# Kernel optimization log

Hardware: AMD Instinct MI355X
Metric: run time of the kernel (lower is better)

Reference implementation:

```python
import jax, jax.numpy as jnp
import numpy as np
from functools import partial

NEG_INF = -1e30

def _alive_mask(x, umbral=0.1):
    # 3x3 max-pool (stride 1, SAME) over channel 0, compare to threshold
    m = x[..., :1]
    pooled = jax.lax.reduce_window(m, NEG_INF, jax.lax.max,
                                   (1, 3, 3, 1), (1, 1, 1, 1), 'SAME')
    return pooled > umbral

def _perception_kernel(canales):
    # identity + sobel-x + sobel-y, fixed (non-learned) depthwise filters
    identidad = np.outer(np.float32([0, 1, 0]), np.float32([0, 1, 0]))
    dx = np.float32(np.outer([1, 2, 1], [-1, 0, 1]) / 8.0)
    dy = dx.T
    k = np.stack([identidad, dx, dy], -1)            # [3,3,3]
    k = np.repeat(k[:, :, None, :], canales + 3, 2)   # [3,3,C+3,3]
    C = canales + 3
    # TF depthwise output channel order: chan*3 + multiplier -> flatten last two dims
    return jnp.asarray(k.reshape(3, 3, 1, C * 3))

def setup_inputs() -> dict:
    key = jax.random.key(0)
    ks = jax.random.split(key, 6)
    B, H, C, HID = 16, 256, 14, 256
    PERC = (C + 3) * 3  # 51
    x = jax.random.uniform(ks[0], (B, H, H, C), dtype=jnp.float32)
    imagen = jax.random.uniform(ks[1], (H, H, 3), dtype=jnp.float32)
    W1 = jax.random.normal(ks[2], (PERC, HID), dtype=jnp.float32) * 0.05
    b1 = jnp.zeros((HID,), dtype=jnp.float32)
    W2 = jax.random.normal(ks[3], (HID, C), dtype=jnp.float32) * 0.05
    b2 = jnp.zeros((C,), dtype=jnp.float32)
    return {"x": x, "imagen": imagen, "W1": W1, "b1": b1, "W2": W2, "b2": b2}

def reference(x, imagen, W1, b1, W2, b2):
    paso = 0.1
    umbral_actualizacion = 0.5
    B = x.shape[0]
    C = x.shape[-1]

    vivos_antes = _alive_mask(x)

    # percibir: concat image, fixed depthwise conv (identity/sobel)
    img_b = jnp.broadcast_to(imagen[None], (B,) + imagen.shape)
    xc = jnp.concatenate([x, img_b], axis=3)                 # [B,H,W,C+3]
    kernel = _perception_kernel(C)                            # [3,3,1,(C+3)*3]
    perc = jax.lax.conv_general_dilated(
        xc, kernel, window_strides=(1, 1), padding='SAME',
        dimension_numbers=('NHWC', 'HWIO', 'NHWC'),
        feature_group_count=C + 3)                            # [B,H,W,51]

    # pointwise MLP (1x1 convs)
    h = jax.nn.relu(jnp.einsum('bhwc,cd->bhwd', perc, W1) + b1)
    dx = (jnp.einsum('bhwd,dc->bhwc', h, W2) + b2) * paso

    # stochastic update mask
    mk = jax.random.fold_in(jax.random.key(0), 1234)
    upd = jax.random.uniform(mk, x[..., :1].shape) <= umbral_actualizacion
    x = x + dx * upd.astype(jnp.float32)

    vivos = jnp.logical_and(vivos_antes, _alive_mask(x))
    return x * vivos.astype(jnp.float32)
```

## Files before the change

kernel.cpp:

```cpp
#include <hip/hip_runtime.h>
#include <stdint.h>

#define C    14
#define CX   17
#define PERC 51
#define HID  256

typedef __attribute__((ext_vector_type(4))) short  bf16x4;
typedef __attribute__((ext_vector_type(8))) short  bf16x8;
typedef __attribute__((ext_vector_type(4))) float  f32x4;
typedef __attribute__((ext_vector_type(8))) unsigned short u16x8;
typedef __attribute__((ext_vector_type(2))) uint32_t u32x2;

__device__ __forceinline__ float bfu(unsigned short u) {
  return __uint_as_float(((uint32_t)u) << 16);
}
__device__ __forceinline__ unsigned short bf16r(float f) {
  uint32_t u = __float_as_uint(f);
  return (unsigned short)((u + 0x7fffu + ((u >> 16) & 1u)) >> 16);
}
__device__ __forceinline__ uint32_t pack2_bf16(float lo, float hi) {
  const uint32_t ul = __float_as_uint(lo) + 0x8000u;
  const uint32_t uh = __float_as_uint(hi) + 0x8000u;
#if __has_builtin(__builtin_amdgcn_perm)
  return __builtin_amdgcn_perm(uh, ul, 0x07060302u);
#else
  return (uh & 0xffff0000u) | (ul >> 16);
#endif
}
__device__ __forceinline__ unsigned short pack1_bf16(float f) {
  return (unsigned short)((__float_as_uint(f) + 0x8000u) >> 16);
}

__device__ __forceinline__ f32x4 mfma32(bf16x8 a, bf16x8 b, f32x4 c) {
  return __builtin_amdgcn_mfma_f32_16x16x32_bf16(a, b, c, 0, 0, 0);
}
#if __has_builtin(__builtin_amdgcn_mfma_f32_16x16x16bf16_1k)
#define HAVE_MFMA16_BUILTIN 1
#endif
__device__ __forceinline__ f32x4 mfma16(bf16x4 a, bf16x4 b, f32x4 c) {
#ifdef HAVE_MFMA16_BUILTIN
  return __builtin_amdgcn_mfma_f32_16x16x16bf16_1k(a, b, c, 0, 0, 0);
#else
  asm volatile("v_mfma_f32_16x16x16_bf16 %0, %1, %2, %0" : "+v"(c) : "v"(a), "v"(b));
  return c;
#endif
}

__device__ __forceinline__ void tf_round(uint32_t& x0, uint32_t& x1, int r) {
  x0 += x1; x1 = (x1 << r) | (x1 >> (32 - r)); x1 ^= x0;
}
__device__ __forceinline__ void threefry2x32(uint32_t k0, uint32_t k1,
                                             uint32_t& x0, uint32_t& x1) {
  const uint32_t ks2 = k0 ^ k1 ^ 0x1BD11BDAu;
  x0 += k0; x1 += k1;
  tf_round(x0,x1,13); tf_round(x0,x1,15); tf_round(x0,x1,26); tf_round(x0,x1,6);
  x0 += k1; x1 += ks2 + 1u;
  tf_round(x0,x1,17); tf_round(x0,x1,29); tf_round(x0,x1,16); tf_round(x0,x1,24);
  x0 += ks2; x1 += k0 + 2u;
  tf_round(x0,x1,13); tf_round(x0,x1,15); tf_round(x0,x1,26); tf_round(x0,x1,6);
  x0 += k0; x1 += k1 + 3u;
  tf_round(x0,x1,17); tf_round(x0,x1,29); tf_round(x0,x1,16); tf_round(x0,x1,24);
  x0 += k1; x1 += ks2 + 4u;
  tf_round(x0,x1,13); tf_round(x0,x1,15); tf_round(x0,x1,26); tf_round(x0,x1,6);
  x0 += ks2; x1 += k0 + 5u;
}
__device__ __forceinline__ float upd_val(uint32_t gpix) {
  uint32_t fk0 = 0u, fk1 = 1234u;
  threefry2x32(0u, 0u, fk0, fk1);
  uint32_t a = 0u, b = gpix;
  threefry2x32(fk0, fk1, a, b);
  const uint32_t bits = a ^ b;
  const float u = __uint_as_float((bits >> 9) | 0x3f800000u) - 1.0f;
  return (u <= 0.5f) ? 1.0f : 0.0f;
}

__global__ void nca_prep(const float* __restrict__ W1, const float* __restrict__ W2,
                         const float* __restrict__ b2,
                         unsigned short* __restrict__ w1fu,
                         unsigned short* __restrict__ w2fu,
                         float* __restrict__ b2p) {
  const int bid = blockIdx.x, t = threadIdx.x;
  if (bid < 64) {
    const int f = bid * 256 + t;
    const int j = f & 7, l = (f >> 3) & 63, k2 = (f >> 9) & 1, mt = f >> 10;
    const int n = mt * 16 + (l & 15);
    const int k = k2 * 32 + ((l >> 4) & 3) * 8 + j;
    const float v = (k < PERC) ? W1[k * HID + n] : 0.0f;
    w1fu[f] = bf16r(v);
  } else if (bid < 80) {
    const int f = (bid - 64) * 256 + t;
    const int j = f & 3, l = (f >> 2) & 63, ks = f >> 8;
    const int co = l & 15;
    const int k = ks * 16 + ((l >> 4) & 3) * 4 + j;
    const float v = (co < C) ? W2[k * C + co] : 0.0f;
    w2fu[f] = bf16r(v);
  } else if (t < 16) {
    b2p[t] = (t < C) ? b2[t] : 0.0f;
  }
}

__global__ __launch_bounds__(256, 2)
void nca_main(const float* __restrict__ x, const float* __restrict__ img,
              const float* __restrict__ b1,
              const unsigned short* __restrict__ w1fu,
              const unsigned short* __restrict__ w2fu,
              const float* __restrict__ b2p,
              float* __restrict__ out, float* __restrict__ plane) {
  __shared__ unsigned short xcs[18 * 18 * 24];
  __shared__ unsigned short Ps[256 * 64];
  __shared__ float updf[256];

  const int t    = threadIdx.x;
  const int bid  = blockIdx.x;
  const int bb   = bid >> 8;
  const int tile = bid & 255;
  const int row0 = (tile >> 4) << 4, col0 = (tile & 15) << 4;

  for (int e = t; e < 324; e += 256) {
    const int r = e / 18, c = e - r * 18;
    const int gr = row0 + r - 1, gc = col0 + c - 1;
    uint32_t w[8]; unsigned short w16;
    if ((unsigned)gr < 256u && (unsigned)gc < 256u) {
      const size_t gp = (size_t)bb * 65536 + (size_t)gr * 256 + gc;
      const float* xp = x + gp * C;
      float v[17];
      #pragma unroll
      for (int k = 0; k < 7; ++k) {
        const float2 f2 = *(const float2*)(xp + 2 * k);
        v[2 * k] = f2.x; v[2 * k + 1] = f2.y;
      }
      const float* ip = img + ((size_t)gr * 256 + gc) * 3;
      v[14] = ip[0]; v[15] = ip[1]; v[16] = ip[2];
      #pragma unroll
      for (int k = 0; k < 8; ++k)
        w[k] = pack2_bf16(v[2 * k], v[2 * k + 1]);
      w16 = pack1_bf16(v[16]);
    } else {
      #pragma unroll
      for (int k = 0; k < 8; ++k) w[k] = 0u;
      w16 = 0;
    }
    uint32_t* d = (uint32_t*)&xcs[e * 24];
    #pragma unroll
    for (int k = 0; k < 8; ++k) d[k] = w[k];
    xcs[e * 24 + 16] = w16;
  }

  {
    const uint32_t g = ((uint32_t)bb * 256u + (uint32_t)(row0 + (t >> 4))) * 256u
                       + (uint32_t)(col0 + (t & 15));
    updf[t] = upd_val(g);
  }
  __syncthreads();

  const int pr = t >> 4, pc = t & 15;
  float pe[64];
  #pragma unroll
  for (int h = 0; h < 2; ++h) {
    u16x8 nb[9];
    #pragma unroll
    for (int i = 0; i < 3; ++i)
      #pragma unroll
      for (int j = 0; j < 3; ++j)
        nb[i * 3 + j] = *(const u16x8*)&xcs[((pr + i) * 18 + (pc + j)) * 24 + h * 8];
    #pragma unroll
    for (int cc = 0; cc < 8; ++cc) {
      const int ch = h * 8 + cc;
      const float a00 = bfu(nb[0][cc]), a01 = bfu(nb[1][cc]), a02 = bfu(nb[2][cc]);
      const float a10 = bfu(nb[3][cc]), a11 = bfu(nb[4][cc]), a12 = bfu(nb[5][cc]);
      const float a20 = bfu(nb[6][cc]), a21 = bfu(nb[7][cc]), a22 = bfu(nb[8][cc]);
      pe[3 * ch + 0] = a11;
      pe[3 * ch + 1] = ((a02 - a00) + 2.0f * (a12 - a10) + (a22 - a20)) * 0.125f;
      pe[3 * ch + 2] = ((a20 - a00) + 2.0f * (a21 - a01) + (a22 - a02)) * 0.125f;
    }
  }
  {
    float a[9];
    #pragma unroll
    for (int i = 0; i < 3; ++i)
      #pragma unroll
      for (int j = 0; j < 3; ++j)
        a[i * 3 + j] = bfu(xcs[((pr + i) * 18 + (pc + j)) * 24 + 16]);
    pe[48] = a[4];
    pe[49] = ((a[2] - a[0]) + 2.0f * (a[5] - a[3]) + (a[8] - a[6])) * 0.125f;
    pe[50] = ((a[6] - a[0]) + 2.0f * (a[7] - a[1]) + (a[8] - a[2])) * 0.125f;
  }
  #pragma unroll
  for (int k = PERC; k < 64; ++k) pe[k] = 0.0f;
  #pragma unroll
  for (int g = 0; g < 8; ++g) {
    uint4 v;
    v.x = pack2_bf16(pe[g * 8 + 0], pe[g * 8 + 1]);
    v.y = pack2_bf16(pe[g * 8 + 2], pe[g * 8 + 3]);
    v.z = pack2_bf16(pe[g * 8 + 4], pe[g * 8 + 5]);
    v.w = pack2_bf16(pe[g * 8 + 6], pe[g * 8 + 7]);
    *(uint4*)&Ps[(t << 6) + ((g ^ (t & 7)) << 3)] = v;
  }
  __syncthreads();

  const int lane = t & 63;
  const int wv   = t >> 6;
  const int wbase = wv << 6;
  const int lg = lane >> 4;
  const int lc = lane & 15;

  bf16x8 bF0[4], bF1[4];
  #pragma unroll
  for (int nt = 0; nt < 4; ++nt) {
    const int pix = wbase + nt * 16 + lc;
    bF0[nt] = *(const bf16x8*)&Ps[(pix << 6) + ((lg ^ (pix & 7)) << 3)];
    bF1[nt] = *(const bf16x8*)&Ps[(pix << 6) + (((4 + lg) ^ (pix & 7)) << 3)];
  }

  f32x4 dxacc[4];
  {
    const float4 b2v = *(const float4*)(b2p + lg * 4);
    #pragma unroll
    for (int nt = 0; nt < 4; ++nt)
      dxacc[nt] = (f32x4){b2v.x, b2v.y, b2v.z, b2v.w};
  }

  #pragma unroll
  for (int nc = 0; nc < 4; ++nc) {
    bf16x8 aF[4][2];
    #pragma unroll
    for (int m4 = 0; m4 < 4; ++m4)
      #pragma unroll
      for (int k2 = 0; k2 < 2; ++k2)
        aF[m4][k2] = *(const bf16x8*)(w1fu + (((((nc * 4 + m4) * 2 + k2) * 64) + lane) << 3));

    f32x4 acc[4][4];
    #pragma unroll
    for (int m4 = 0; m4 < 4; ++m4) {
      const float4 b1v = *(const float4*)(b1 + nc * 64 + m4 * 16 + lg * 4);
      #pragma unroll
      for (int nt = 0; nt < 4; ++nt)
        acc[m4][nt] = (f32x4){b1v.x, b1v.y, b1v.z, b1v.w};
    }

    #pragma unroll
    for (int nt = 0; nt < 4; ++nt) {
      #pragma unroll
      for (int m4 = 0; m4 < 4; ++m4) acc[m4][nt] = mfma32(aF[m4][0], bF0[nt], acc[m4][nt]);
      #pragma unroll
      for (int m4 = 0; m4 < 4; ++m4) acc[m4][nt] = mfma32(aF[m4][1], bF1[nt], acc[m4][nt]);
    }

    #pragma unroll
    for (int m4 = 0; m4 < 4; ++m4) {
      const bf16x4 wf = *(const bf16x4*)(w2fu + ((((nc * 4 + m4) * 64) + lane) << 2));
      #pragma unroll
      for (int nt = 0; nt < 4; ++nt) {
        u32x2 pw;
        pw.x = pack2_bf16(fmaxf(acc[m4][nt][0], 0.0f), fmaxf(acc[m4][nt][1], 0.0f));
        pw.y = pack2_bf16(fmaxf(acc[m4][nt][2], 0.0f), fmaxf(acc[m4][nt][3], 0.0f));
        dxacc[nt] = mfma16(wf, __builtin_bit_cast(bf16x4, pw), dxacc[nt]);
      }
    }
  }
#ifndef HAVE_MFMA16_BUILTIN
  asm volatile("s_nop 7\n\ts_nop 7" :::);
#endif

  #pragma unroll
  for (int nt = 0; nt < 4; ++nt) {
    const int pix = wbase + nt * 16 + lc;
    const float sc = 0.1f * updf[pix];
    const int gr = row0 + (pix >> 4), gc = col0 + (pix & 15);
    const size_t gp = (size_t)bb * 65536 + (size_t)gr * 256 + gc;
    const float* xp = x + gp * C + lg * 4;
    float* op = out + gp * C + lg * 4;
    const f32x4 d = dxacc[nt];
    if (lg < 3) {
      const float2 u0 = *(const float2*)xp;
      const float2 u1 = *(const float2*)(xp + 2);
      const float r0 = u0.x + d[0] * sc, r1 = u0.y + d[1] * sc;
      const float r2 = u1.x + d[2] * sc, r3 = u1.y + d[3] * sc;
      *(float2*)op = make_float2(r0, r1);
      *(float2*)(op + 2) = make_float2(r2, r3);
      if (lg == 0) plane[gp] = r0;
    } else {
      const float2 u0 = *(const float2*)xp;
      *(float2*)op = make_float2(u0.x + d[0] * sc, u0.y + d[1] * sc);
    }
  }
}

__global__ __launch_bounds__(256)
void nca_mask(const float* __restrict__ x, const float* __restrict__ plane,
              float* __restrict__ out) {
  __shared__ float sN[18 * 18];
  __shared__ float sO[18 * 18];
  const int t    = threadIdx.x;
  const int bid  = blockIdx.x;
  const int bb   = bid >> 8;
  const int tile = bid & 255;
  const int row0 = (tile >> 4) << 4, col0 = (tile & 15) << 4;

  for (int e = t; e < 18 * 18; e += 256) {
    const int r = e / 18, c = e - r * 18;
    const int gr = row0 + r - 1, gc = col0 + c - 1;
    float vn = 0.0f, vo = 0.0f;
    if ((unsigned)gr < 256u && (unsigned)gc < 256u) {
      const size_t gp = ((size_t)bb * 256 + gr) * 256 + gc;
      vn = plane[gp];
      vo = x[gp * C];
    }
    sN[e] = vn; sO[e] = vo;
  }
  __syncthreads();

  const int pr = t >> 4, pc = t & 15;
  float mn = -1e30f, mo = -1e30f;
  #pragma unroll
  for (int i = 0; i < 3; ++i)
    #pragma unroll
    for (int j = 0; j < 3; ++j) {
      mn = fmaxf(mn, sN[(pr + i) * 18 + pc + j]);
      mo = fmaxf(mo, sO[(pr + i) * 18 + pc + j]);
    }
  const bool alive = (mo > 0.1f) && (mn > 0.1f);
  if (!alive) {
    const size_t gp = ((size_t)bb * 256 + row0 + pr) * 256 + col0 + pc;
    float* __restrict__ o = out + gp * C;
    const float2 z = make_float2(0.0f, 0.0f);
    #pragma unroll
    for (int k = 0; k < 7; ++k) ((float2*)o)[k] = z;
  }
}

extern "C" void kernel_launch(void* const* d_in, const int* in_sizes, int n_in,
                              void* d_out, int out_size, void* d_ws, size_t ws_size,
                              hipStream_t stream) {
  const float* x  = (const float*)d_in[0];
  const float* im = (const float*)d_in[1];
  const float* W1 = (const float*)d_in[2];
  const float* b1 = (const float*)d_in[3];
  const float* W2 = (const float*)d_in[4];
  const float* b2 = (const float*)d_in[5];
  float* out   = (float*)d_out;
  float* plane = (float*)d_ws;
  unsigned short* w1fu = (unsigned short*)((char*)d_ws + 4194304);
  unsigned short* w2fu = (unsigned short*)((char*)d_ws + 4194304 + 32768);
  float* b2p = (float*)((char*)d_ws + 4194304 + 32768 + 8192);

  nca_prep<<<81,   256, 0, stream>>>(W1, W2, b2, w1fu, w2fu, b2p);
  nca_main<<<4096, 256, 0, stream>>>(x, im, b1, w1fu, w2fu, b2p, out, plane);
  nca_mask<<<4096, 256, 0, stream>>>(x, plane, out);
}
```

Before: 96.75 us.

## Fold b1 into W1 via constant-one column and alias LDS buffers

The first-layer bias is folded into the padded K column of W1 (perception channel 51 is set to 1), so accumulators start at zero and the per-chunk b1 global loads go away. The halo tile and perception-matrix LDS buffers are overlaid in a union, separated by an extra barrier, which cuts shared memory per block. Launch bounds are raised from 2 to 4 blocks per SIMD/CU to raise occupancy. This trades bias precision (now bf16) and may cause register spills under the tighter register budget.

```diff
diff --git a/kernel.cpp b/kernel.cpp
--- a/kernel.cpp
+++ b/kernel.cpp
@@ -75,8 +75,8 @@
   return (u <= 0.5f) ? 1.0f : 0.0f;
 }
 
-__global__ void nca_prep(const float* __restrict__ W1, const float* __restrict__ W2,
-                         const float* __restrict__ b2,
+__global__ void nca_prep(const float* __restrict__ W1, const float* __restrict__ b1,
+                         const float* __restrict__ W2, const float* __restrict__ b2,
                          unsigned short* __restrict__ w1fu,
                          unsigned short* __restrict__ w2fu,
                          float* __restrict__ b2p) {
@@ -86,7 +86,9 @@
     const int j = f & 7, l = (f >> 3) & 63, k2 = (f >> 9) & 1, mt = f >> 10;
     const int n = mt * 16 + (l & 15);
     const int k = k2 * 32 + ((l >> 4) & 3) * 8 + j;
-    const float v = (k < PERC) ? W1[k * HID + n] : 0.0f;
+    float v = 0.0f;
+    if (k < PERC)       v = W1[k * HID + n];
+    else if (k == PERC) v = b1[n];
     w1fu[f] = bf16r(v);
   } else if (bid < 80) {
     const int f = (bid - 64) * 256 + t;
@@ -100,15 +102,16 @@
   }
 }
 
-__global__ __launch_bounds__(256, 2)
+__global__ __launch_bounds__(256, 4)
 void nca_main(const float* __restrict__ x, const float* __restrict__ img,
-              const float* __restrict__ b1,
               const unsigned short* __restrict__ w1fu,
               const unsigned short* __restrict__ w2fu,
               const float* __restrict__ b2p,
               float* __restrict__ out, float* __restrict__ plane) {
-  __shared__ unsigned short xcs[18 * 18 * 24];
-  __shared__ unsigned short Ps[256 * 64];
+  __shared__ union {
+    unsigned short xcs[18 * 18 * 24];
+    unsigned short Ps[256 * 64];
+  } sh;
   __shared__ float updf[256];
 
   const int t    = threadIdx.x;
@@ -141,10 +144,10 @@
       for (int k = 0; k < 8; ++k) w[k] = 0u;
       w16 = 0;
     }
-    uint32_t* d = (uint32_t*)&xcs[e * 24];
+    uint32_t* d = (uint32_t*)&sh.xcs[e * 24];
     #pragma unroll
     for (int k = 0; k < 8; ++k) d[k] = w[k];
-    xcs[e * 24 + 16] = w16;
+    sh.xcs[e * 24 + 16] = w16;
   }
 
   {
@@ -163,7 +166,7 @@
     for (int i = 0; i < 3; ++i)
       #pragma unroll
       for (int j = 0; j < 3; ++j)
-        nb[i * 3 + j] = *(const u16x8*)&xcs[((pr + i) * 18 + (pc + j)) * 24 + h * 8];
+        nb[i * 3 + j] = *(const u16x8*)&sh.xcs[((pr + i) * 18 + (pc + j)) * 24 + h * 8];
     #pragma unroll
     for (int cc = 0; cc < 8; ++cc) {
       const int ch = h * 8 + cc;
@@ -181,13 +184,17 @@
     for (int i = 0; i < 3; ++i)
       #pragma unroll
       for (int j = 0; j < 3; ++j)
-        a[i * 3 + j] = bfu(xcs[((pr + i) * 18 + (pc + j)) * 24 + 16]);
+        a[i * 3 + j] = bfu(sh.xcs[((pr + i) * 18 + (pc + j)) * 24 + 16]);
     pe[48] = a[4];
     pe[49] = ((a[2] - a[0]) + 2.0f * (a[5] - a[3]) + (a[8] - a[6])) * 0.125f;
     pe[50] = ((a[6] - a[0]) + 2.0f * (a[7] - a[1]) + (a[8] - a[2])) * 0.125f;
   }
-  #pragma unroll
-  for (int k = PERC; k < 64; ++k) pe[k] = 0.0f;
+  pe[51] = 1.0f;
+  #pragma unroll
+  for (int k = 52; k < 64; ++k) pe[k] = 0.0f;
+
+  __syncthreads();
+
   #pragma unroll
   for (int g = 0; g < 8; ++g) {
     uint4 v;
@@ -195,7 +202,7 @@
     v.y = pack2_bf16(pe[g * 8 + 2], pe[g * 8 + 3]);
     v.z = pack2_bf16(pe[g * 8 + 4], pe[g * 8 + 5]);
     v.w = pack2_bf16(pe[g * 8 + 6], pe[g * 8 + 7]);
-    *(uint4*)&Ps[(t << 6) + ((g ^ (t & 7)) << 3)] = v;
+    *(uint4*)&sh.Ps[(t << 6) + ((g ^ (t & 7)) << 3)] = v;
   }
   __syncthreads();
 
@@ -209,8 +216,8 @@
   #pragma unroll
   for (int nt = 0; nt < 4; ++nt) {
     const int pix = wbase + nt * 16 + lc;
-    bF0[nt] = *(const bf16x8*)&Ps[(pix << 6) + ((lg ^ (pix & 7)) << 3)];
-    bF1[nt] = *(const bf16x8*)&Ps[(pix << 6) + (((4 + lg) ^ (pix & 7)) << 3)];
+    bF0[nt] = *(const bf16x8*)&sh.Ps[(pix << 6) + ((lg ^ (pix & 7)) << 3)];
+    bF1[nt] = *(const bf16x8*)&sh.Ps[(pix << 6) + (((4 + lg) ^ (pix & 7)) << 3)];
   }
 
   f32x4 dxacc[4];
@@ -232,12 +239,10 @@
 
     f32x4 acc[4][4];
     #pragma unroll
-    for (int m4 = 0; m4 < 4; ++m4) {
-      const float4 b1v = *(const float4*)(b1 + nc * 64 + m4 * 16 + lg * 4);
+    for (int m4 = 0; m4 < 4; ++m4)
       #pragma unroll
       for (int nt = 0; nt < 4; ++nt)
-        acc[m4][nt] = (f32x4){b1v.x, b1v.y, b1v.z, b1v.w};
-    }
+        acc[m4][nt] = (f32x4){0.0f, 0.0f, 0.0f, 0.0f};
 
     #pragma unroll
     for (int nt = 0; nt < 4; ++nt) {
@@ -345,7 +350,7 @@
   unsigned short* w2fu = (unsigned short*)((char*)d_ws + 4194304 + 32768);
   float* b2p = (float*)((char*)d_ws + 4194304 + 32768 + 8192);
 
-  nca_prep<<<81,   256, 0, stream>>>(W1, W2, b2, w1fu, w2fu, b2p);
-  nca_main<<<4096, 256, 0, stream>>>(x, im, b1, w1fu, w2fu, b2p, out, plane);
+  nca_prep<<<81,   256, 0, stream>>>(W1, b1, W2, b2, w1fu, w2fu, b2p);
+  nca_main<<<4096, 256, 0, stream>>>(x, im, w1fu, w2fu, b2p, out, plane);
   nca_mask<<<4096, 256, 0, stream>>>(x, plane, out);
 }
```

After: 93.89 us. 1.03x faster.
